# Kernel tuning notes

Measured on AMD Instinct MI355X. Metric: run time of the kernel, lower is better.

The kernel has to match this reference:

```python
import jax, jax.numpy as jnp
import numpy as np

N = 100000   # nodes
E = 600000   # directed edges (no self loops)
T = 128      # n_timestamps
DIMS = [128, 64, 32, 16]  # get_layer_dims(128, 3, 0.5)


def _glorot(key, din, dout):
    lim = float(np.sqrt(6.0 / (din + dout)))
    return jax.random.uniform(key, (din, dout), jnp.float32, -lim, lim)


def setup_inputs() -> dict:
    key = jax.random.key(0)
    ks = jax.random.split(key, 16)
    row = jax.random.randint(ks[0], (E,), 0, N, dtype=jnp.int32)
    off = jax.random.randint(ks[1], (E,), 1, N, dtype=jnp.int32)
    col = (row + off) % N  # guarantees no self loops
    edge_index = jnp.stack([row, col])
    x = jax.random.normal(ks[2], (N, T), dtype=jnp.float32)
    enc = [(DIMS[0], DIMS[1]), (DIMS[1], DIMS[2]), (DIMS[2], DIMS[3])]
    dec = [(DIMS[3], DIMS[2]), (DIMS[2], DIMS[1]), (DIMS[1], DIMS[0])]
    inp = {"x": x, "edge_index": edge_index}
    for i, (di, do) in enumerate(enc):
        inp[f"We{i+1}"] = _glorot(ks[3 + i], di, do)
        inp[f"be{i+1}"] = 0.01 * jax.random.normal(ks[6 + i], (do,), jnp.float32)
    for i, (di, do) in enumerate(dec):
        inp[f"Wd{i+1}"] = _glorot(ks[9 + i], di, do)
        inp[f"bd{i+1}"] = 0.01 * jax.random.normal(ks[12 + i], (do,), jnp.float32)
    return inp


def _with_self_loops(edge_index, n):
    ar = jnp.arange(n, dtype=edge_index.dtype)
    row = jnp.concatenate([edge_index[0], ar])
    col = jnp.concatenate([edge_index[1], ar])
    return row, col


def _deg_inv_sqrt(w, col, n):
    deg = jax.ops.segment_sum(w, col, num_segments=n)
    return jnp.where(deg > 0, jax.lax.rsqrt(deg), 0.0)


def _smooth_norm(edge_index, n):
    # gcn_norm: A_hat = A + I (fill 1), sym normalize D^-1/2 A_hat D^-1/2
    row, col = _with_self_loops(edge_index, n)
    w = jnp.ones(row.shape[0], jnp.float32)
    dinv = _deg_inv_sqrt(w, col, n)
    return row, col, dinv[row] * w * dinv[col]


def _sharp_norm(edge_index, n):
    # gcn_sharp: A_hat = -A + 2I, D_hat from (A + 2I), norm = D^-1/2 A_hat D^-1/2
    row, col = _with_self_loops(edge_index, n)
    e = edge_index.shape[1]
    wA = jnp.concatenate([-jnp.ones(e, jnp.float32), 2.0 * jnp.ones(n, jnp.float32)])
    wD = jnp.concatenate([jnp.ones(e, jnp.float32), 2.0 * jnp.ones(n, jnp.float32)])
    dinv = _deg_inv_sqrt(wD, col, n)
    return row, col, dinv[row] * wA * dinv[col]


def _conv(x, W, b, row, col, ew, n):
    # x -> lin -> gather source, scale by edge weight, scatter-add to target, + bias
    h = x @ W
    out = jax.ops.segment_sum(ew[:, None] * h[row], col, num_segments=n)
    return out + b


def reference(x, edge_index, We1, be1, We2, be2, We3, be3,
              Wd1, bd1, Wd2, bd2, Wd3, bd3):
    n = x.shape[0]
    sr, sc, sw = _smooth_norm(edge_index, n)   # encoder ('smooth')
    hr, hc, hw = _sharp_norm(edge_index, n)    # decoder ('sharp')
    # encoder: conv+ReLU x3
    h = jax.nn.relu(_conv(x, We1, be1, sr, sc, sw, n))
    h = jax.nn.relu(_conv(h, We2, be2, sr, sc, sw, n))
    z = jax.nn.relu(_conv(h, We3, be3, sr, sc, sw, n))
    # decoder: conv+ReLU x2, final conv without ReLU
    h = jax.nn.relu(_conv(z, Wd1, bd1, hr, hc, hw, n))
    h = jax.nn.relu(_conv(h, Wd2, bd2, hr, hc, hw, n))
    o = _conv(h, Wd3, bd3, hr, hc, hw, n)
    return o
```

## Files before the change

### kernel.cpp

```cpp
#include <hip/hip_runtime.h>


static inline int ceil_div(int a, int b) { return (a + b - 1) / b; }

#define SCAN_BLK 256
#define NBINS 128

typedef _Float16 f16;
typedef _Float16 f16x8 __attribute__((ext_vector_type(8)));
typedef float f32x4 __attribute__((ext_vector_type(4)));


__global__ void deg_kernel(const int* __restrict__ col, int* __restrict__ deg, int E) {
    int e = blockIdx.x * blockDim.x + threadIdx.x;
    if (e < E) atomicAdd(&deg[col[e]], 1);
}


__global__ void hist_kernel(const int* __restrict__ deg, int* __restrict__ blockhist, int n) {
    __shared__ int lh[NBINS];
    if (threadIdx.x < NBINS) lh[threadIdx.x] = 0;
    __syncthreads();
    int i = blockIdx.x * SCAN_BLK + threadIdx.x;
    if (i < n) {
        int d = deg[i]; if (d >= NBINS) d = NBINS - 1;
        atomicAdd(&lh[d], 1);
    }
    __syncthreads();
    if (threadIdx.x < NBINS) blockhist[blockIdx.x * NBINS + threadIdx.x] = lh[threadIdx.x];
}

__global__ void binscan_kernel(int* __restrict__ blockhist, int* __restrict__ bintot, int nb) {
    __shared__ int s[512];
    int bin = blockIdx.x, t = threadIdx.x;
    int v = (t < nb) ? blockhist[t * NBINS + bin] : 0;
    s[t] = v;
    __syncthreads();
    for (int st = 1; st < 512; st <<= 1) {
        int a = (t >= st) ? s[t - st] : 0;
        __syncthreads();
        s[t] += a;
        __syncthreads();
    }
    if (t < nb) blockhist[t * NBINS + bin] = s[t] - v;
    if (t == 0) bintot[bin] = s[511];
}

__global__ void base_scan_kernel(const int* __restrict__ bintot, int* __restrict__ binbase,
                                 int* __restrict__ edgebase) {
    __shared__ int s[NBINS], se[NBINS];
    int t = threadIdx.x;
    int v = bintot[t];
    int ve = v * t;
    s[t] = v; se[t] = ve;
    __syncthreads();
    for (int st = 1; st < NBINS; st <<= 1) {
        int a = (t >= st) ? s[t - st] : 0;
        int ae = (t >= st) ? se[t - st] : 0;
        __syncthreads();
        s[t] += a; se[t] += ae;
        __syncthreads();
    }
    binbase[t] = s[t] - v;
    edgebase[t] = se[t] - ve;
}

__global__ void place_kernel(const int* __restrict__ deg, const int* __restrict__ blockhist,
                             const int* __restrict__ binbase, int* __restrict__ order,
                             int* __restrict__ slotof, int n) {
    __shared__ int lh[NBINS];
    if (threadIdx.x < NBINS) lh[threadIdx.x] = 0;
    __syncthreads();
    int i = blockIdx.x * SCAN_BLK + threadIdx.x;
    if (i < n) {
        int d = deg[i]; if (d >= NBINS) d = NBINS - 1;
        int r = atomicAdd(&lh[d], 1);
        int slot = binbase[d] + blockhist[blockIdx.x * NBINS + d] + r;
        order[slot] = i;
        slotof[i] = slot;
    }
}

__global__ void dinvp_offs_kernel(const int* __restrict__ deg, const int* __restrict__ order,
                                  const int* __restrict__ binbase, const int* __restrict__ edgebase,
                                  float* __restrict__ dinv_s, float* __restrict__ dinv_h,
                                  int* __restrict__ offs, int* __restrict__ cursor, int n, int E) {
    int s = blockIdx.x * blockDim.x + threadIdx.x;
    if (s < n) {
        int dd = deg[order[s]];
        float d = (float)dd;
        dinv_s[s] = rsqrtf(d + 1.0f);
        dinv_h[s] = rsqrtf(d + 2.0f);
        int o = edgebase[dd] + dd * (s - binbase[dd]);
        offs[s] = o;
        cursor[s] = o;
        if (s == 0) offs[n] = E;
    }
}

__global__ void csr_fill_kernel(const int* __restrict__ row, const int* __restrict__ col,
                                const int* __restrict__ slotof, int* __restrict__ cursor,
                                int* __restrict__ src, int E) {
    int e = blockIdx.x * blockDim.x + threadIdx.x;
    if (e >= E) return;
    int cs = slotof[col[e]];
    int p = atomicAdd(&cursor[cs], 1);
    src[p] = slotof[row[e]];
}


struct WPtrs { const float* p[6]; };

__global__ void wsplit_kernel(WPtrs wp, f16* __restrict__ wt_hi, f16* __restrict__ wt_lo) {
    const int din[6]  = {128, 64, 32, 16, 32, 64};
    const int dout[6] = {64, 32, 16, 32, 64, 128};
    const int off[6]  = {0, 8192, 10240, 10752, 11264, 13312};
    int t = blockIdx.x * blockDim.x + threadIdx.x;
    if (t >= 21504) return;
    int l = 0;
    while (l < 5 && t >= off[l + 1]) ++l;
    int idx = t - off[l];
    int c = idx / din[l], k = idx - c * din[l];
    float a = wp.p[l][k * dout[l] + c];
    f16 hi = (f16)a;
    f16 lo = (f16)(a - (float)hi);
    wt_hi[t] = hi;
    wt_lo[t] = lo;
}


#define M_PLAIN 0
#define M_SMOOTH 1
#define M_SHARP 2
#define M_SHARP_RELU 3

template <int DIN, int DOUT, int WAVES, int MODE, bool ADD_BIAS, bool RELU_OUT,
          bool SCALE_ROW, bool IN_PERM, bool OUT_PERM, bool OUT_F32>
__global__ __launch_bounds__(WAVES * 64) void gemm_fused(
        const float* __restrict__ Af, const f16* __restrict__ U,
        const f16* __restrict__ Wth, const f16* __restrict__ Wtl,
        const float* __restrict__ gbias, const float* __restrict__ gdinv,
        const int* __restrict__ offs, const int* __restrict__ srcv,
        const float* __restrict__ bias, const float* __restrict__ rs,
        const int* __restrict__ map, float* __restrict__ outf,
        f16* __restrict__ outh, int n) {
    constexpr int THREADS = WAVES * 64;
    constexpr int BM  = WAVES * 16;
    constexpr int KC  = (DIN >= 64) ? 64 : DIN;
    constexpr int KCP = (KC < 32) ? 32 : KC;
    constexpr int NKC = DIN / KC;
    constexpr int KS  = KCP / 32;
    constexpr int NT  = DOUT / 16;
    constexpr int LDB = KCP * 2 + 16;
    constexpr int AG  = KCP / 8;
    __shared__ __align__(16) unsigned char Asm[(size_t)BM * LDB];

    const int row0 = blockIdx.x * BM;
    const int lane = threadIdx.x & 63;
    const int wave = __builtin_amdgcn_readfirstlane((int)(threadIdx.x >> 6));
    const int l15 = lane & 15, lhi = lane >> 4;

    f32x4 acc[NT];
#pragma unroll
    for (int t = 0; t < NT; ++t) acc[t] = (f32x4){0.f, 0.f, 0.f, 0.f};

    for (int kc = 0; kc < NKC; ++kc) {
        const int kofs = kc * KC;
        if (kc > 0) __syncthreads();
        for (int i = threadIdx.x; i < BM * AG; i += THREADS) {
            int r = i / AG, j = i % AG;
            f16x8 hv = {0, 0, 0, 0, 0, 0, 0, 0};
            int gr = row0 + r;
            if (gr < n && j * 8 < KC) {
                const int k8 = kofs + j * 8;
                if (MODE == M_PLAIN) {
                    int ar = IN_PERM ? map[gr] : gr;
                    float4 v0 = *(const float4*)(Af + (size_t)ar * DIN + k8);
                    float4 v1 = *(const float4*)(Af + (size_t)ar * DIN + k8 + 4);
                    hv[0] = (f16)v0.x; hv[1] = (f16)v0.y; hv[2] = (f16)v0.z; hv[3] = (f16)v0.w;
                    hv[4] = (f16)v1.x; hv[5] = (f16)v1.y; hv[6] = (f16)v1.z; hv[7] = (f16)v1.w;
                } else {
                    f16x8 s8 = *(const f16x8*)(U + (size_t)gr * DIN + k8);
                    float sf[8], g[8];
#pragma unroll
                    for (int q = 0; q < 8; ++q) {
                        sf[q] = (float)s8[q];
                        if (MODE == M_SHARP_RELU) sf[q] = fmaxf(sf[q], 0.f);
                        g[q] = 0.f;
                    }
                    int e = offs[gr], e1 = offs[gr + 1];
                    for (; e + 4 <= e1; e += 4) {
                        int r0 = srcv[e], r1 = srcv[e + 1], r2 = srcv[e + 2], r3 = srcv[e + 3];
                        f16x8 t0 = *(const f16x8*)(U + (size_t)r0 * DIN + k8);
                        f16x8 t1 = *(const f16x8*)(U + (size_t)r1 * DIN + k8);
                        f16x8 t2 = *(const f16x8*)(U + (size_t)r2 * DIN + k8);
                        f16x8 t3 = *(const f16x8*)(U + (size_t)r3 * DIN + k8);
#pragma unroll
                        for (int q = 0; q < 8; ++q) {
                            float a0 = (float)t0[q], a1 = (float)t1[q];
                            float a2 = (float)t2[q], a3 = (float)t3[q];
                            if (MODE == M_SHARP_RELU) {
                                a0 = fmaxf(a0, 0.f); a1 = fmaxf(a1, 0.f);
                                a2 = fmaxf(a2, 0.f); a3 = fmaxf(a3, 0.f);
                            }
                            g[q] += (a0 + a1) + (a2 + a3);
                        }
                    }
                    for (; e < e1; ++e) {
                        f16x8 t0 = *(const f16x8*)(U + (size_t)srcv[e] * DIN + k8);
#pragma unroll
                        for (int q = 0; q < 8; ++q) {
                            float a0 = (float)t0[q];
                            if (MODE == M_SHARP_RELU) a0 = fmaxf(a0, 0.f);
                            g[q] += a0;
                        }
                    }
                    float dv = gdinv[gr];
#pragma unroll
                    for (int q = 0; q < 8; ++q) {
                        float v;
                        if (MODE == M_SMOOTH) {
                            v = fmaf(dv, g[q] + sf[q], gbias[k8 + q]);
                            v = fmaxf(v, 0.f);
                        } else {
                            v = dv * (2.f * sf[q] - g[q]);
                        }
                        hv[q] = (f16)v;
                    }
                }
            }
            *(f16x8*)(Asm + (size_t)r * LDB + j * 16) = hv;
        }
        __syncthreads();

#pragma unroll
        for (int ks = 0; ks < KS; ++ks) {
            f16x8 a = *(const f16x8*)(Asm + (size_t)(wave * 16 + l15) * LDB + ks * 64 + lhi * 16);
#pragma unroll
            for (int t = 0; t < NT; ++t) {
                const f16* wb = Wth + (size_t)(t * 16 + l15) * DIN + kofs + ks * 32 + lhi * 8;
                const f16* wc = Wtl + (size_t)(t * 16 + l15) * DIN + kofs + ks * 32 + lhi * 8;
                f16x8 bh = *(const f16x8*)wb;
                f16x8 bl = *(const f16x8*)wc;
                acc[t] = __builtin_amdgcn_mfma_f32_16x16x32_f16(a, bh, acc[t], 0, 0, 0);
                acc[t] = __builtin_amdgcn_mfma_f32_16x16x32_f16(a, bl, acc[t], 0, 0, 0);
            }
        }
    }

    const int rbase = row0 + wave * 16 + (lhi << 2);
    float rsv[4]; int om[4];
#pragma unroll
    for (int r = 0; r < 4; ++r) {
        int row = rbase + r;
        bool ok = row < n;
        rsv[r] = (SCALE_ROW && ok) ? rs[row] : 1.0f;
        om[r] = ok ? (OUT_PERM ? map[row] : row) : -1;
    }
#pragma unroll
    for (int t = 0; t < NT; ++t) {
        int colb = t * 16 + l15;
        float b = ADD_BIAS ? bias[colb] : 0.f;
#pragma unroll
        for (int r = 0; r < 4; ++r) {
            if (om[r] < 0) continue;
            float v = acc[t][r] + b;
            if (RELU_OUT) v = fmaxf(v, 0.f);
            if (SCALE_ROW) v *= rsv[r];
            if (OUT_F32) outf[(size_t)om[r] * DOUT + colb] = v;
            else         outh[(size_t)om[r] * DOUT + colb] = (f16)v;
        }
    }
}


__global__ __launch_bounds__(256) void gather16(
        const f16* __restrict__ u, const int* __restrict__ offs,
        const int* __restrict__ src, const float* __restrict__ dinv,
        const float* __restrict__ ps, const float* __restrict__ bias,
        f16* __restrict__ out, int n) {
    int idx = blockIdx.x * blockDim.x + threadIdx.x;
    int node = idx >> 1;
    if (node >= n) return;
    int d8 = (idx & 1) * 8;

    f16x8 s8 = *(const f16x8*)(u + (size_t)node * 16 + d8);
    float g[8];
#pragma unroll
    for (int q = 0; q < 8; ++q) g[q] = 0.f;
    int e = offs[node], e1 = offs[node + 1];
    for (; e + 4 <= e1; e += 4) {
        int r0 = src[e], r1 = src[e + 1], r2 = src[e + 2], r3 = src[e + 3];
        f16x8 t0 = *(const f16x8*)(u + (size_t)r0 * 16 + d8);
        f16x8 t1 = *(const f16x8*)(u + (size_t)r1 * 16 + d8);
        f16x8 t2 = *(const f16x8*)(u + (size_t)r2 * 16 + d8);
        f16x8 t3 = *(const f16x8*)(u + (size_t)r3 * 16 + d8);
#pragma unroll
        for (int q = 0; q < 8; ++q)
            g[q] += ((float)t0[q] + (float)t1[q]) + ((float)t2[q] + (float)t3[q]);
    }
    for (; e < e1; ++e) {
        f16x8 t0 = *(const f16x8*)(u + (size_t)src[e] * 16 + d8);
#pragma unroll
        for (int q = 0; q < 8; ++q) g[q] += (float)t0[q];
    }
    float dv = dinv[node], p = ps[node];
    f16x8 o;
#pragma unroll
    for (int q = 0; q < 8; ++q) {
        float v = p * (fmaf(dv, g[q] + (float)s8[q], bias[d8 + q]));
        o[q] = (f16)v;
    }
    *(f16x8*)(out + (size_t)node * 16 + d8) = o;
}


extern "C" void kernel_launch(void* const* d_in, const int* in_sizes, int n_in,
                              void* d_out, int out_size, void* d_ws, size_t ws_size,
                              hipStream_t stream) {
    const int T = 128;
    const int n = in_sizes[0] / T;
    const int E = in_sizes[1] / 2;

    const float* x   = (const float*)d_in[0];
    const int* eidx  = (const int*)d_in[1];
    const int* row   = eidx;
    const int* col   = eidx + E;
    const float* We1 = (const float*)d_in[2];
    const float* be1 = (const float*)d_in[3];
    const float* We2 = (const float*)d_in[4];
    const float* be2 = (const float*)d_in[5];
    const float* We3 = (const float*)d_in[6];
    const float* be3 = (const float*)d_in[7];
    const float* Wd1 = (const float*)d_in[8];
    const float* bd1 = (const float*)d_in[9];
    const float* Wd2 = (const float*)d_in[10];
    const float* bd2 = (const float*)d_in[11];
    const float* Wd3 = (const float*)d_in[12];
    const float* bd3 = (const float*)d_in[13];
    float* out = (float*)d_out;

    char* base = (char*)d_ws;
    int*   deg      = (int*)base;   base += (size_t)n * 4;
    int*   offs     = (int*)base;   base += (size_t)(n + 4) * 4;
    int*   cursor   = (int*)base;   base += (size_t)(n + 4) * 4;
    int*   bhist    = (int*)base;   base += (size_t)512 * NBINS * 4;
    int*   bintot   = (int*)base;   base += (size_t)NBINS * 4;
    int*   binbase  = (int*)base;   base += (size_t)NBINS * 4;
    int*   edgebase = (int*)base;   base += (size_t)NBINS * 4;
    int*   order    = (int*)base;   base += (size_t)n * 4;
    int*   slotof   = (int*)base;   base += (size_t)n * 4;
    float* dinv_s   = (float*)base; base += (size_t)n * 4;
    float* dinv_h   = (float*)base; base += (size_t)n * 4;
    int*   src      = (int*)base;   base += (size_t)E * 4;
    f16*   wt_hi    = (f16*)base;   base += (size_t)21504 * 2 + 64;
    f16*   wt_lo    = (f16*)base;   base += (size_t)21504 * 2 + 64;
    f16*   bufA     = (f16*)base;   base += (size_t)n * 64 * 2;
    f16*   bufB     = (f16*)base;   base += (size_t)n * 64 * 2;
    (void)ws_size;

    const int BLK = 256;
    const int nhb = ceil_div(n, SCAN_BLK);

    hipMemsetAsync(deg, 0, (size_t)n * 4, stream);
    deg_kernel<<<ceil_div(E, BLK), BLK, 0, stream>>>(col, deg, E);

    hist_kernel<<<nhb, SCAN_BLK, 0, stream>>>(deg, bhist, n);
    binscan_kernel<<<NBINS, 512, 0, stream>>>(bhist, bintot, nhb);
    base_scan_kernel<<<1, NBINS, 0, stream>>>(bintot, binbase, edgebase);
    place_kernel<<<nhb, SCAN_BLK, 0, stream>>>(deg, bhist, binbase, order, slotof, n);
    dinvp_offs_kernel<<<ceil_div(n, BLK), BLK, 0, stream>>>(
        deg, order, binbase, edgebase, dinv_s, dinv_h, offs, cursor, n, E);
    csr_fill_kernel<<<ceil_div(E, BLK), BLK, 0, stream>>>(row, col, slotof, cursor, src, E);

    WPtrs wp; wp.p[0] = We1; wp.p[1] = We2; wp.p[2] = We3;
    wp.p[3] = Wd1; wp.p[4] = Wd2; wp.p[5] = Wd3;
    wsplit_kernel<<<ceil_div(21504, BLK), BLK, 0, stream>>>(wp, wt_hi, wt_lo);

    const int ggrid = ceil_div(n, 128);

    gemm_fused<128, 64, 8, M_PLAIN, false, false, true, true, false, false>
        <<<ggrid, 512, 0, stream>>>(
        x, nullptr, wt_hi + 0, wt_lo + 0, nullptr, nullptr, nullptr, nullptr,
        nullptr, dinv_s, order, nullptr, bufA, n);

    gemm_fused<64, 32, 8, M_SMOOTH, false, false, true, false, false, false>
        <<<ggrid, 512, 0, stream>>>(
        nullptr, bufA, wt_hi + 8192, wt_lo + 8192, be1, dinv_s, offs, src,
        nullptr, dinv_s, nullptr, nullptr, bufB, n);

    gemm_fused<32, 16, 8, M_SMOOTH, false, false, true, false, false, false>
        <<<ggrid, 512, 0, stream>>>(
        nullptr, bufB, wt_hi + 10240, wt_lo + 10240, be2, dinv_s, offs, src,
        nullptr, dinv_s, nullptr, nullptr, bufA, n);

    gather16<<<ceil_div(n * 2, BLK), BLK, 0, stream>>>(
        bufA, offs, src, dinv_s, dinv_h, be3, bufB, n);

    gemm_fused<16, 32, 8, M_SHARP_RELU, true, true, true, false, false, false>
        <<<ggrid, 512, 0, stream>>>(
        nullptr, bufB, wt_hi + 10752, wt_lo + 10752, nullptr, dinv_h, offs, src,
        bd1, dinv_h, nullptr, nullptr, bufA, n);

    gemm_fused<32, 64, 8, M_SHARP, true, true, true, false, false, false>
        <<<ggrid, 512, 0, stream>>>(
        nullptr, bufA, wt_hi + 11264, wt_lo + 11264, nullptr, dinv_h, offs, src,
        bd2, dinv_h, nullptr, nullptr, bufB, n);

    gemm_fused<64, 128, 8, M_SHARP, true, false, false, false, true, true>
        <<<ggrid, 512, 0, stream>>>(
        nullptr, bufB, wt_hi + 13312, wt_lo + 13312, nullptr, dinv_h, offs, src,
        bd3, nullptr, order, out, nullptr, n);
}
```

Measured before the change: 270.7 us.

## Stage full A rows once and stage split weights through LDS per K-chunk

The fused gather+GEMM kernel now builds the whole K extent of each A row tile in LDS in a single pass, instead of alternating gather and MFMA per 64-wide chunk. Weight hi/lo halves are staged into padded LDS tiles per 32-wide K chunk, and MFMA B operands are read from LDS instead of from global memory. This removes the per-chunk barrier between gather and compute, and shares weight loads across all waves in the block. In exchange it uses more LDS per block, which can lower occupancy for the DIN=128 layers, and it adds barriers for every weight chunk.

```diff
diff --git a/kernel.cpp b/kernel.cpp
--- a/kernel.cpp
+++ b/kernel.cpp
@@ -145,15 +145,17 @@
         const int* __restrict__ map, float* __restrict__ outf,
         f16* __restrict__ outh, int n) {
     constexpr int THREADS = WAVES * 64;
-    constexpr int BM  = WAVES * 16;
-    constexpr int KC  = (DIN >= 64) ? 64 : DIN;
-    constexpr int KCP = (KC < 32) ? 32 : KC;
-    constexpr int NKC = DIN / KC;
-    constexpr int KS  = KCP / 32;
-    constexpr int NT  = DOUT / 16;
-    constexpr int LDB = KCP * 2 + 16;
-    constexpr int AG  = KCP / 8;
-    __shared__ __align__(16) unsigned char Asm[(size_t)BM * LDB];
+    constexpr int BM   = WAVES * 16;
+    constexpr int KROW = (DIN < 32) ? 32 : DIN;
+    constexpr int NKC  = KROW / 32;
+    constexpr int NT   = DOUT / 16;
+    constexpr int LDA  = KROW * 2 + 16;
+    constexpr int LDW  = 80;
+    constexpr int AGF  = KROW / 8;
+    __shared__ __align__(16) unsigned char lds[(size_t)BM * LDA + (size_t)2 * DOUT * LDW];
+    unsigned char* Asm = lds;
+    unsigned char* Wh  = lds + (size_t)BM * LDA;
+    unsigned char* Wl  = Wh + (size_t)DOUT * LDW;
 
     const int row0 = blockIdx.x * BM;
     const int lane = threadIdx.x & 63;
@@ -164,87 +166,93 @@
 #pragma unroll
     for (int t = 0; t < NT; ++t) acc[t] = (f32x4){0.f, 0.f, 0.f, 0.f};
 
-    for (int kc = 0; kc < NKC; ++kc) {
-        const int kofs = kc * KC;
-        if (kc > 0) __syncthreads();
-        for (int i = threadIdx.x; i < BM * AG; i += THREADS) {
-            int r = i / AG, j = i % AG;
-            f16x8 hv = {0, 0, 0, 0, 0, 0, 0, 0};
-            int gr = row0 + r;
-            if (gr < n && j * 8 < KC) {
-                const int k8 = kofs + j * 8;
-                if (MODE == M_PLAIN) {
-                    int ar = IN_PERM ? map[gr] : gr;
-                    float4 v0 = *(const float4*)(Af + (size_t)ar * DIN + k8);
-                    float4 v1 = *(const float4*)(Af + (size_t)ar * DIN + k8 + 4);
-                    hv[0] = (f16)v0.x; hv[1] = (f16)v0.y; hv[2] = (f16)v0.z; hv[3] = (f16)v0.w;
-                    hv[4] = (f16)v1.x; hv[5] = (f16)v1.y; hv[6] = (f16)v1.z; hv[7] = (f16)v1.w;
-                } else {
-                    f16x8 s8 = *(const f16x8*)(U + (size_t)gr * DIN + k8);
-                    float sf[8], g[8];
+    for (int i = threadIdx.x; i < BM * AGF; i += THREADS) {
+        int r = i / AGF, j = i % AGF;
+        f16x8 hv = {0, 0, 0, 0, 0, 0, 0, 0};
+        int gr = row0 + r;
+        const int k8 = j * 8;
+        if (gr < n && k8 < DIN) {
+            if (MODE == M_PLAIN) {
+                int ar = IN_PERM ? map[gr] : gr;
+                float4 v0 = *(const float4*)(Af + (size_t)ar * DIN + k8);
+                float4 v1 = *(const float4*)(Af + (size_t)ar * DIN + k8 + 4);
+                hv[0] = (f16)v0.x; hv[1] = (f16)v0.y; hv[2] = (f16)v0.z; hv[3] = (f16)v0.w;
+                hv[4] = (f16)v1.x; hv[5] = (f16)v1.y; hv[6] = (f16)v1.z; hv[7] = (f16)v1.w;
+            } else {
+                f16x8 s8 = *(const f16x8*)(U + (size_t)gr * DIN + k8);
+                float sf[8], g[8];
+#pragma unroll
+                for (int q = 0; q < 8; ++q) {
+                    sf[q] = (float)s8[q];
+                    if (MODE == M_SHARP_RELU) sf[q] = fmaxf(sf[q], 0.f);
+                    g[q] = 0.f;
+                }
+                int e = offs[gr], e1 = offs[gr + 1];
+                for (; e + 4 <= e1; e += 4) {
+                    int r0 = srcv[e], r1 = srcv[e + 1], r2 = srcv[e + 2], r3 = srcv[e + 3];
+                    f16x8 t0 = *(const f16x8*)(U + (size_t)r0 * DIN + k8);
+                    f16x8 t1 = *(const f16x8*)(U + (size_t)r1 * DIN + k8);
+                    f16x8 t2 = *(const f16x8*)(U + (size_t)r2 * DIN + k8);
+                    f16x8 t3 = *(const f16x8*)(U + (size_t)r3 * DIN + k8);
 #pragma unroll
                     for (int q = 0; q < 8; ++q) {
-                        sf[q] = (float)s8[q];
-                        if (MODE == M_SHARP_RELU) sf[q] = fmaxf(sf[q], 0.f);
-                        g[q] = 0.f;
-                    }
-                    int e = offs[gr], e1 = offs[gr + 1];
-                    for (; e + 4 <= e1; e += 4) {
-                        int r0 = srcv[e], r1 = srcv[e + 1], r2 = srcv[e + 2], r3 = srcv[e + 3];
-                        f16x8 t0 = *(const f16x8*)(U + (size_t)r0 * DIN + k8);
-                        f16x8 t1 = *(const f16x8*)(U + (size_t)r1 * DIN + k8);
-                        f16x8 t2 = *(const f16x8*)(U + (size_t)r2 * DIN + k8);
-                        f16x8 t3 = *(const f16x8*)(U + (size_t)r3 * DIN + k8);
-#pragma unroll
-                        for (int q = 0; q < 8; ++q) {
-                            float a0 = (float)t0[q], a1 = (float)t1[q];
-                            float a2 = (float)t2[q], a3 = (float)t3[q];
-                            if (MODE == M_SHARP_RELU) {
-                                a0 = fmaxf(a0, 0.f); a1 = fmaxf(a1, 0.f);
-                                a2 = fmaxf(a2, 0.f); a3 = fmaxf(a3, 0.f);
-                            }
-                            g[q] += (a0 + a1) + (a2 + a3);
+                        float a0 = (float)t0[q], a1 = (float)t1[q];
+                        float a2 = (float)t2[q], a3 = (float)t3[q];
+                        if (MODE == M_SHARP_RELU) {
+                            a0 = fmaxf(a0, 0.f); a1 = fmaxf(a1, 0.f);
+                            a2 = fmaxf(a2, 0.f); a3 = fmaxf(a3, 0.f);
                         }
-                    }
-                    for (; e < e1; ++e) {
-                        f16x8 t0 = *(const f16x8*)(U + (size_t)srcv[e] * DIN + k8);
-#pragma unroll
-                        for (int q = 0; q < 8; ++q) {
-                            float a0 = (float)t0[q];
-                            if (MODE == M_SHARP_RELU) a0 = fmaxf(a0, 0.f);
-                            g[q] += a0;
-                        }
-                    }
-                    float dv = gdinv[gr];
-#pragma unroll
-                    for (int q = 0; q < 8; ++q) {
-                        float v;
-                        if (MODE == M_SMOOTH) {
-                            v = fmaf(dv, g[q] + sf[q], gbias[k8 + q]);
-                            v = fmaxf(v, 0.f);
-                        } else {
-                            v = dv * (2.f * sf[q] - g[q]);
-                        }
-                        hv[q] = (f16)v;
+                        g[q] += (a0 + a1) + (a2 + a3);
                     }
                 }
+                for (; e < e1; ++e) {
+                    f16x8 t0 = *(const f16x8*)(U + (size_t)srcv[e] * DIN + k8);
+#pragma unroll
+                    for (int q = 0; q < 8; ++q) {
+                        float a0 = (float)t0[q];
+                        if (MODE == M_SHARP_RELU) a0 = fmaxf(a0, 0.f);
+                        g[q] += a0;
+                    }
+                }
+                float dv = gdinv[gr];
+#pragma unroll
+                for (int q = 0; q < 8; ++q) {
+                    float v;
+                    if (MODE == M_SMOOTH) {
+                        v = fmaf(dv, g[q] + sf[q], gbias[k8 + q]);
+                        v = fmaxf(v, 0.f);
+                    } else {
+                        v = dv * (2.f * sf[q] - g[q]);
+                    }
+                    hv[q] = (f16)v;
+                }
             }
-            *(f16x8*)(Asm + (size_t)r * LDB + j * 16) = hv;
+        }
+        *(f16x8*)(Asm + (size_t)r * LDA + j * 16) = hv;
+    }
+
+    for (int kc = 0; kc < NKC; ++kc) {
+        const int kofs = kc * 32;
+        if (kc > 0) __syncthreads();
+        for (int i = threadIdx.x; i < DOUT * 4; i += THREADS) {
+            int c = i / 4, j = i % 4;
+            f16x8 h8 = {0, 0, 0, 0, 0, 0, 0, 0}, l8 = {0, 0, 0, 0, 0, 0, 0, 0};
+            if (kofs + j * 8 < DIN) {
+                h8 = *(const f16x8*)(Wth + (size_t)c * DIN + kofs + j * 8);
+                l8 = *(const f16x8*)(Wtl + (size_t)c * DIN + kofs + j * 8);
+            }
+            *(f16x8*)(Wh + (size_t)c * LDW + j * 16) = h8;
+            *(f16x8*)(Wl + (size_t)c * LDW + j * 16) = l8;
         }
         __syncthreads();
 
-#pragma unroll
-        for (int ks = 0; ks < KS; ++ks) {
-            f16x8 a = *(const f16x8*)(Asm + (size_t)(wave * 16 + l15) * LDB + ks * 64 + lhi * 16);
-#pragma unroll
-            for (int t = 0; t < NT; ++t) {
-                const f16* wb = Wth + (size_t)(t * 16 + l15) * DIN + kofs + ks * 32 + lhi * 8;
-                const f16* wc = Wtl + (size_t)(t * 16 + l15) * DIN + kofs + ks * 32 + lhi * 8;
-                f16x8 bh = *(const f16x8*)wb;
-                f16x8 bl = *(const f16x8*)wc;
-                acc[t] = __builtin_amdgcn_mfma_f32_16x16x32_f16(a, bh, acc[t], 0, 0, 0);
-                acc[t] = __builtin_amdgcn_mfma_f32_16x16x32_f16(a, bl, acc[t], 0, 0, 0);
-            }
+        f16x8 a = *(const f16x8*)(Asm + (size_t)(wave * 16 + l15) * LDA + kc * 64 + lhi * 16);
+#pragma unroll
+        for (int t = 0; t < NT; ++t) {
+            f16x8 bh = *(const f16x8*)(Wh + (size_t)(t * 16 + l15) * LDW + lhi * 16);
+            f16x8 bl = *(const f16x8*)(Wl + (size_t)(t * 16 + l15) * LDW + lhi * 16);
+            acc[t] = __builtin_amdgcn_mfma_f32_16x16x32_f16(a, bh, acc[t], 0, 0, 0);
+            acc[t] = __builtin_amdgcn_mfma_f32_16x16x32_f16(a, bl, acc[t], 0, 0, 0);
         }
     }
 
```

Result: faster. 222.2 us (-17.9%).
